# Kernel optimization log

Measured on AMD Instinct MI355X. Metric: run time of the kernel, lower is better.

## Reference

```python
import jax, jax.numpy as jnp
import numpy as np

NFFT = 512
SHIFT = 160
EPS = 1e-07
LOG10 = float(np.log(10.0))


def setup_inputs() -> dict:
    key = jax.random.key(0)
    x = jax.random.normal(key, (32, 1, 96512), dtype=jnp.float32)
    n = np.arange(NFFT)
    ang = 2.0 * np.pi * np.outer(n, n) / NFFT  # [k, n]
    W_real = np.cos(ang).astype(np.float32)
    W_imag = (-np.sin(ang)).astype(np.float32)
    return {"x": x, "W_real": jnp.asarray(W_real), "W_imag": jnp.asarray(W_imag)}


def reference(x, W_real, W_imag):
    # x: [B, C, T]; W_real/W_imag: [nfft, nfft] DFT basis (kernel k over taps n)
    B, C, T = x.shape
    n_frames = (T - NFFT) // SHIFT + 1
    # strided frame extraction == Conv1d(stride=SHIFT, kernel=NFFT) unfolding
    idx = jnp.arange(n_frames)[:, None] * SHIFT + jnp.arange(NFFT)[None, :]  # [F, N]
    frames = x[:, :, idx]  # [B, C, F, N]
    real = jnp.einsum('bcfn,kn->bckf', frames, W_real)  # [B, C, nfft, F]
    imag = jnp.einsum('bcfn,kn->bckf', frames, W_imag)
    # mode == 'log': log10 of magnitude spectrogram (with epsilon inside sqrt)
    fft = jnp.log(jnp.sqrt(real * real + imag * imag + EPS)) / LOG10
    fft = fft[:, :, : NFFT // 2, :]  # keep lower half of spectrum
    # normalize_feature: zero-mean, unit-std over frequency axis (biased std)
    mean = jnp.mean(fft, axis=2, keepdims=True)
    std = jnp.std(fft, axis=2, keepdims=True)
    return (fft - mean) / (std + EPS)
```

## Files before the change

kernel.cpp:

```cpp
#include <hip/hip_runtime.h>
#include <stdint.h>

#define TLEN    96512
#define NBATCH  32
#define KOUT    256
#define SHIFT   160
#define NFRAMES 601
#define FT      76
#define NTILES  8
#define NKS     16
#define EPSF    1e-7f

typedef _Float16 f16;
typedef _Float16 half8 __attribute__((ext_vector_type(8)));
typedef float f32x16 __attribute__((ext_vector_type(16)));

#define SPAN       ((FT - 1) * SHIFT + 256)
#define UNITS      (SPAN / 8)
#define PLANE_B    24576
#define LDS_RED    104768
#define LDS_STAT   (LDS_RED + 6144)
#define LDS_TOTAL  (LDS_STAT + 768)

__global__ __launch_bounds__(256) void split_w_kernel(
    const float* __restrict__ Wr, const float* __restrict__ Wi,
    f16* __restrict__ wsW)
{
    int id   = blockIdx.x * 256 + threadIdx.x;
    int lane = id & 63;
    int hl   = (id >> 6) & 1;
    int ri   = (id >> 7) & 1;
    int ks   = (id >> 8) & 15;
    int J    = (id >> 12) & 3;
    int par  = (id >> 14) & 1;
    int l31  = lane & 31, lhi = lane >> 5;
    int k = 2 * (J * 32 + l31) + par;
    int n = ks * 16 + lhi * 8;
    const float* src = (ri ? Wi : Wr) + k * 512 + n;
    f16 v[8];
    #pragma unroll
    for (int j = 0; j < 8; ++j) {
        float xv = src[j];
        f16 h = (f16)xv;
        v[j] = hl ? (f16)(xv - (float)h) : h;
    }
    int c = ((par * 4 + J) * 16 + ks) * 4 + ri * 2 + hl;
    *(half8*)(wsW + (size_t)c * 512 + (l31 * 2 + lhi) * 8) = *(half8*)v;
}

__device__ __forceinline__ void load_a(half8 (&a)[2][2],
    const f16* __restrict__ wsW, int par, int J, int laneoff, int ks)
{
    #pragma unroll
    for (int ri = 0; ri < 2; ++ri)
      #pragma unroll
      for (int hl = 0; hl < 2; ++hl) {
          int c = ((par * 4 + J) * 16 + ks) * 4 + ri * 2 + hl;
          a[ri][hl] = *(const half8*)(wsW + (size_t)c * 512 + laneoff);
      }
}

__device__ __forceinline__ void load_b(half8 (&bb)[3][2],
    const char* smem, int par, int l31, int lhi, int ks)
{
    #pragma unroll
    for (int nf = 0; nf < 3; ++nf)
      #pragma unroll
      for (int hl = 0; hl < 2; ++hl) {
          int u  = (nf * 32 + l31) * 20 + ks * 2 + lhi;
          int up = u ^ ((u >> 3) & 7);
          bb[nf][hl] = *(const half8*)(smem + (par * 2 + hl) * PLANE_B + up * 16);
      }
}

__device__ __forceinline__ void do_mfma(f32x16 (&acc)[3][2],
    const half8 (&a)[2][2], const half8 (&bb)[3][2])
{
    #pragma unroll
    for (int nf = 0; nf < 3; ++nf)
      #pragma unroll
      for (int ri = 0; ri < 2; ++ri) {
          acc[nf][ri] = __builtin_amdgcn_mfma_f32_32x32x16_f16(
              a[ri][0], bb[nf][0], acc[nf][ri], 0, 0, 0);
          acc[nf][ri] = __builtin_amdgcn_mfma_f32_32x32x16_f16(
              a[ri][0], bb[nf][1], acc[nf][ri], 0, 0, 0);
          acc[nf][ri] = __builtin_amdgcn_mfma_f32_32x32x16_f16(
              a[ri][1], bb[nf][0], acc[nf][ri], 0, 0, 0);
      }
}

__global__ __launch_bounds__(512, 2) void dft_mfma_kernel(
    const f16* __restrict__ wsW, const float* __restrict__ x,
    float* __restrict__ out)
{
    __shared__ uint4 smem4[LDS_TOTAL / 16];
    char* smem = (char*)smem4;

    const int tid  = threadIdx.x;
    const int lane = tid & 63;
    const int w    = tid >> 6;
    const int l31  = lane & 31;
    const int lhi  = lane >> 5;
    const int b    = blockIdx.y;
    const int f0   = blockIdx.x * FT;
    const int par  = w & 1;
    const int J    = w >> 1;
    const int laneoff = (l31 * 2 + lhi) * 8;

    half8 a0[2][2], a1[2][2], b0[3][2], b1[3][2];
    load_a(a0, wsW, par, J, laneoff, 0);

    {
        const float* __restrict__ xb = x + (size_t)b * TLEN;
        const int t0 = f0 * SHIFT;
        for (int u = tid; u < UNITS; u += 512) {
            int t = t0 + u * 8;
            float va[8], vb[8];
            if (t + 264 <= TLEN) {
                float4 p0 = *(const float4*)(xb + t);
                float4 p1 = *(const float4*)(xb + t + 4);
                float4 q0 = *(const float4*)(xb + t + 256);
                float4 q1 = *(const float4*)(xb + t + 260);
                va[0]=p0.x; va[1]=p0.y; va[2]=p0.z; va[3]=p0.w;
                va[4]=p1.x; va[5]=p1.y; va[6]=p1.z; va[7]=p1.w;
                vb[0]=q0.x; vb[1]=q0.y; vb[2]=q0.z; vb[3]=q0.w;
                vb[4]=q1.x; vb[5]=q1.y; vb[6]=q1.z; vb[7]=q1.w;
            } else {
                #pragma unroll
                for (int j = 0; j < 8; ++j) {
                    int ta = t + j, tb = t + 256 + j;
                    va[j] = (ta < TLEN) ? xb[ta] : 0.f;
                    vb[j] = (tb < TLEN) ? xb[tb] : 0.f;
                }
            }
            f16 eh[8], el[8], oh[8], ol[8];
            #pragma unroll
            for (int j = 0; j < 8; ++j) {
                float E = va[j] + vb[j], O = va[j] - vb[j];
                eh[j] = (f16)E; el[j] = (f16)(E - (float)eh[j]);
                oh[j] = (f16)O; ol[j] = (f16)(O - (float)oh[j]);
            }
            int up = u ^ ((u >> 3) & 7);
            *(half8*)(smem + 0 * PLANE_B + up * 16) = *(half8*)eh;
            *(half8*)(smem + 1 * PLANE_B + up * 16) = *(half8*)el;
            *(half8*)(smem + 2 * PLANE_B + up * 16) = *(half8*)oh;
            *(half8*)(smem + 3 * PLANE_B + up * 16) = *(half8*)ol;
        }
    }
    __syncthreads();

    f32x16 acc[3][2] = {};
    load_b(b0, smem, par, l31, lhi, 0);

    #pragma unroll
    for (int ks2 = 0; ks2 < NKS; ks2 += 2) {
        load_a(a1, wsW, par, J, laneoff, ks2 + 1);
        load_b(b1, smem, par, l31, lhi, ks2 + 1);
        do_mfma(acc, a0, b0);
        int k2 = (ks2 + 2 < NKS) ? ks2 + 2 : NKS - 1;
        load_a(a0, wsW, par, J, laneoff, k2);
        load_b(b0, smem, par, l31, lhi, k2);
        do_mfma(acc, a1, b1);
    }

    const float C = 0.15051499783199057f;
    float lg[3][16];
    float s1[3] = {0.f, 0.f, 0.f}, s2[3] = {0.f, 0.f, 0.f};
    #pragma unroll
    for (int nf = 0; nf < 3; ++nf)
      #pragma unroll
      for (int r = 0; r < 16; ++r) {
          float re = acc[nf][0][r], im = acc[nf][1][r];
          float lv = C * __log2f(re * re + im * im + EPSF);
          lg[nf][r] = lv;
          s1[nf] += lv;
          s2[nf] += lv * lv;
      }
    #pragma unroll
    for (int nf = 0; nf < 3; ++nf) {
        s1[nf] += __shfl_xor(s1[nf], 32);
        s2[nf] += __shfl_xor(s2[nf], 32);
    }
    float2* red = (float2*)(smem + LDS_RED);
    if (lane < 32) {
        #pragma unroll
        for (int nf = 0; nf < 3; ++nf)
            red[(w * 3 + nf) * 32 + l31] = make_float2(s1[nf], s2[nf]);
    }
    __syncthreads();
    float* stat = (float*)(smem + LDS_STAT);
    if (tid < 96) {
        float S1 = 0.f, S2 = 0.f;
        int nf = tid >> 5, c = tid & 31;
        #pragma unroll
        for (int ww = 0; ww < 8; ++ww) {
            float2 p = red[(ww * 3 + nf) * 32 + c];
            S1 += p.x; S2 += p.y;
        }
        float mean = S1 * (1.f / 256.f);
        float var  = fmaxf(S2 * (1.f / 256.f) - mean * mean, 0.f);
        stat[tid]      = mean;
        stat[96 + tid] = 1.f / (__builtin_sqrtf(var) + EPSF);
    }
    __syncthreads();

    #pragma unroll
    for (int nf = 0; nf < 3; ++nf) {
        int fl = nf * 32 + l31;
        int f  = f0 + fl;
        if (fl >= FT || f >= NFRAMES) continue;
        float mean = stat[fl], rstd = stat[96 + fl];
        #pragma unroll
        for (int r = 0; r < 16; ++r) {
            int k = 2 * (J * 32 + (r & 3) + 8 * (r >> 2) + 4 * lhi) + par;
            out[((size_t)b * KOUT + k) * NFRAMES + f] = (lg[nf][r] - mean) * rstd;
        }
    }
}

extern "C" void kernel_launch(void* const* d_in, const int* in_sizes, int n_in,
                              void* d_out, int out_size, void* d_ws, size_t ws_size,
                              hipStream_t stream) {
    const float* x  = (const float*)d_in[0];
    const float* Wr = (const float*)d_in[1];
    const float* Wi = (const float*)d_in[2];
    float* out = (float*)d_out;

    f16* wsW = (f16*)d_ws;

    split_w_kernel<<<128, 256, 0, stream>>>(Wr, Wi, wsW);

    dim3 grid(NTILES, NBATCH);
    dft_mfma_kernel<<<grid, 512, 0, stream>>>(wsW, x, out);
}
```

Baseline: 33.92 us.

## Shrink frame tile to 32 for more blocks and occupancy, simplify MFMA loop

The frame tile per block drops from 76 (three 32-wide N fragments, padded to 96) to 32, so the grid grows from 8x32 to 19x32 blocks. LDS per block shrinks and launch bounds rise to 4 blocks per CU. The aim is better CU coverage with less padding waste, plus higher occupancy to hide latency. The explicit double-buffered A/B prefetch is replaced by a simple unrolled loop with s_setprio around the MFMAs, and split_w is restructured so each thread writes both the high and low halves. In exchange, each block reloads the A (W) fragments for fewer frames, so W traffic grows and there is more overlapping x staging per frame.

```diff
diff --git a/kernel.cpp b/kernel.cpp
--- a/kernel.cpp
+++ b/kernel.cpp
@@ -6,8 +6,8 @@
 #define KOUT    256
 #define SHIFT   160
 #define NFRAMES 601
-#define FT      76
-#define NTILES  8
+#define FT      32
+#define NTILES  19
 #define NKS     16
 #define EPSF    1e-7f
 
@@ -17,79 +17,59 @@
 
 #define SPAN       ((FT - 1) * SHIFT + 256)
 #define UNITS      (SPAN / 8)
-#define PLANE_B    24576
-#define LDS_RED    104768
-#define LDS_STAT   (LDS_RED + 6144)
-#define LDS_TOTAL  (LDS_STAT + 768)
+#define PLANE_B    (UNITS * 16)
+#define LDS_RED    (4 * PLANE_B)
+#define LDS_STAT   (LDS_RED + 2048)
+#define LDS_TOTAL  (LDS_STAT + 256)
 
 __global__ __launch_bounds__(256) void split_w_kernel(
     const float* __restrict__ Wr, const float* __restrict__ Wi,
     f16* __restrict__ wsW)
 {
-    int id   = blockIdx.x * 256 + threadIdx.x;
-    int lane = id & 63;
-    int hl   = (id >> 6) & 1;
-    int ri   = (id >> 7) & 1;
-    int ks   = (id >> 8) & 15;
-    int J    = (id >> 12) & 3;
-    int par  = (id >> 14) & 1;
-    int l31  = lane & 31, lhi = lane >> 5;
-    int k = 2 * (J * 32 + l31) + par;
-    int n = ks * 16 + lhi * 8;
-    const float* src = (ri ? Wi : Wr) + k * 512 + n;
-    f16 v[8];
+    int id = blockIdx.x * 256 + threadIdx.x;
+    int n8 = id & 31;
+    int k  = (id >> 5) & 255;
+    int ri = (id >> 13) & 1;
+    const float* src = (ri ? Wi : Wr) + k * 512 + n8 * 8;
+    f16 h[8], l[8];
     #pragma unroll
     for (int j = 0; j < 8; ++j) {
-        float xv = src[j];
-        f16 h = (f16)xv;
-        v[j] = hl ? (f16)(xv - (float)h) : h;
-    }
-    int c = ((par * 4 + J) * 16 + ks) * 4 + ri * 2 + hl;
-    *(half8*)(wsW + (size_t)c * 512 + (l31 * 2 + lhi) * 8) = *(half8*)v;
+        float v = src[j];
+        h[j] = (f16)v;
+        l[j] = (f16)(v - (float)h[j]);
+    }
+    int par = k & 1, kk = k >> 1;
+    int l31 = kk & 31, J = kk >> 5;
+    int ks  = n8 >> 1, lhi = n8 & 1;
+    int c0  = ((par * 4 + J) * 16 + ks) * 4 + ri * 2;
+    size_t off = (size_t)(l31 * 2 + lhi) * 8;
+    *(half8*)(wsW + (size_t)(c0 + 0) * 512 + off) = *(half8*)h;
+    *(half8*)(wsW + (size_t)(c0 + 1) * 512 + off) = *(half8*)l;
 }
 
 __device__ __forceinline__ void load_a(half8 (&a)[2][2],
-    const f16* __restrict__ wsW, int par, int J, int laneoff, int ks)
+    const f16* __restrict__ wsW, int cbase, int laneoff, int ks)
 {
     #pragma unroll
     for (int ri = 0; ri < 2; ++ri)
       #pragma unroll
       for (int hl = 0; hl < 2; ++hl) {
-          int c = ((par * 4 + J) * 16 + ks) * 4 + ri * 2 + hl;
+          int c = cbase + ks * 4 + ri * 2 + hl;
           a[ri][hl] = *(const half8*)(wsW + (size_t)c * 512 + laneoff);
       }
 }
 
-__device__ __forceinline__ void load_b(half8 (&bb)[3][2],
-    const char* smem, int par, int l31, int lhi, int ks)
-{
-    #pragma unroll
-    for (int nf = 0; nf < 3; ++nf)
-      #pragma unroll
-      for (int hl = 0; hl < 2; ++hl) {
-          int u  = (nf * 32 + l31) * 20 + ks * 2 + lhi;
-          int up = u ^ ((u >> 3) & 7);
-          bb[nf][hl] = *(const half8*)(smem + (par * 2 + hl) * PLANE_B + up * 16);
-      }
-}
-
-__device__ __forceinline__ void do_mfma(f32x16 (&acc)[3][2],
-    const half8 (&a)[2][2], const half8 (&bb)[3][2])
-{
-    #pragma unroll
-    for (int nf = 0; nf < 3; ++nf)
-      #pragma unroll
-      for (int ri = 0; ri < 2; ++ri) {
-          acc[nf][ri] = __builtin_amdgcn_mfma_f32_32x32x16_f16(
-              a[ri][0], bb[nf][0], acc[nf][ri], 0, 0, 0);
-          acc[nf][ri] = __builtin_amdgcn_mfma_f32_32x32x16_f16(
-              a[ri][0], bb[nf][1], acc[nf][ri], 0, 0, 0);
-          acc[nf][ri] = __builtin_amdgcn_mfma_f32_32x32x16_f16(
-              a[ri][1], bb[nf][0], acc[nf][ri], 0, 0, 0);
-      }
-}
-
-__global__ __launch_bounds__(512, 2) void dft_mfma_kernel(
+__device__ __forceinline__ void load_b(half8 (&bb)[2],
+    const char* smem, int par, int ubase, int ks)
+{
+    int u  = ubase + ks * 2;
+    int up = u ^ ((u >> 3) & 3);
+    #pragma unroll
+    for (int hl = 0; hl < 2; ++hl)
+        bb[hl] = *(const half8*)(smem + (par * 2 + hl) * PLANE_B + up * 16);
+}
+
+__global__ __launch_bounds__(512, 4) void dft_mfma_kernel(
     const f16* __restrict__ wsW, const float* __restrict__ x,
     float* __restrict__ out)
 {
@@ -105,10 +85,9 @@
     const int f0   = blockIdx.x * FT;
     const int par  = w & 1;
     const int J    = w >> 1;
+    const int cbase   = (par * 4 + J) * 64;
     const int laneoff = (l31 * 2 + lhi) * 8;
-
-    half8 a0[2][2], a1[2][2], b0[3][2], b1[3][2];
-    load_a(a0, wsW, par, J, laneoff, 0);
+    const int ubase   = l31 * 20 + lhi;
 
     {
         const float* __restrict__ xb = x + (size_t)b * TLEN;
@@ -140,7 +119,7 @@
                 eh[j] = (f16)E; el[j] = (f16)(E - (float)eh[j]);
                 oh[j] = (f16)O; ol[j] = (f16)(O - (float)oh[j]);
             }
-            int up = u ^ ((u >> 3) & 7);
+            int up = u ^ ((u >> 3) & 3);
             *(half8*)(smem + 0 * PLANE_B + up * 16) = *(half8*)eh;
             *(half8*)(smem + 1 * PLANE_B + up * 16) = *(half8*)el;
             *(half8*)(smem + 2 * PLANE_B + up * 16) = *(half8*)oh;
@@ -149,71 +128,67 @@
     }
     __syncthreads();
 
-    f32x16 acc[3][2] = {};
-    load_b(b0, smem, par, l31, lhi, 0);
-
-    #pragma unroll
-    for (int ks2 = 0; ks2 < NKS; ks2 += 2) {
-        load_a(a1, wsW, par, J, laneoff, ks2 + 1);
-        load_b(b1, smem, par, l31, lhi, ks2 + 1);
-        do_mfma(acc, a0, b0);
-        int k2 = (ks2 + 2 < NKS) ? ks2 + 2 : NKS - 1;
-        load_a(a0, wsW, par, J, laneoff, k2);
-        load_b(b0, smem, par, l31, lhi, k2);
-        do_mfma(acc, a1, b1);
+    f32x16 acc[2] = {};
+
+    #pragma unroll 4
+    for (int ks = 0; ks < NKS; ++ks) {
+        half8 a[2][2], bb[2];
+        load_a(a, wsW, cbase, laneoff, ks);
+        load_b(bb, smem, par, ubase, ks);
+
+        __builtin_amdgcn_s_setprio(1);
+        #pragma unroll
+        for (int ri = 0; ri < 2; ++ri) {
+            acc[ri] = __builtin_amdgcn_mfma_f32_32x32x16_f16(
+                a[ri][0], bb[0], acc[ri], 0, 0, 0);
+            acc[ri] = __builtin_amdgcn_mfma_f32_32x32x16_f16(
+                a[ri][0], bb[1], acc[ri], 0, 0, 0);
+            acc[ri] = __builtin_amdgcn_mfma_f32_32x32x16_f16(
+                a[ri][1], bb[0], acc[ri], 0, 0, 0);
+        }
+        __builtin_amdgcn_s_setprio(0);
     }
 
     const float C = 0.15051499783199057f;
-    float lg[3][16];
-    float s1[3] = {0.f, 0.f, 0.f}, s2[3] = {0.f, 0.f, 0.f};
-    #pragma unroll
-    for (int nf = 0; nf < 3; ++nf)
-      #pragma unroll
-      for (int r = 0; r < 16; ++r) {
-          float re = acc[nf][0][r], im = acc[nf][1][r];
-          float lv = C * __log2f(re * re + im * im + EPSF);
-          lg[nf][r] = lv;
-          s1[nf] += lv;
-          s2[nf] += lv * lv;
-      }
-    #pragma unroll
-    for (int nf = 0; nf < 3; ++nf) {
-        s1[nf] += __shfl_xor(s1[nf], 32);
-        s2[nf] += __shfl_xor(s2[nf], 32);
-    }
+    float lg[16];
+    float s1 = 0.f, s2 = 0.f;
+    #pragma unroll
+    for (int r = 0; r < 16; ++r) {
+        float re = acc[0][r], im = acc[1][r];
+        float lv = C * __log2f(re * re + im * im + EPSF);
+        lg[r] = lv;
+        s1 += lv;
+        s2 += lv * lv;
+    }
+    s1 += __shfl_xor(s1, 32);
+    s2 += __shfl_xor(s2, 32);
+
     float2* red = (float2*)(smem + LDS_RED);
-    if (lane < 32) {
-        #pragma unroll
-        for (int nf = 0; nf < 3; ++nf)
-            red[(w * 3 + nf) * 32 + l31] = make_float2(s1[nf], s2[nf]);
-    }
+    if (lane < 32)
+        red[w * 32 + l31] = make_float2(s1, s2);
     __syncthreads();
     float* stat = (float*)(smem + LDS_STAT);
-    if (tid < 96) {
+    if (tid < 32) {
         float S1 = 0.f, S2 = 0.f;
-        int nf = tid >> 5, c = tid & 31;
         #pragma unroll
         for (int ww = 0; ww < 8; ++ww) {
-            float2 p = red[(ww * 3 + nf) * 32 + c];
+            float2 p = red[ww * 32 + tid];
             S1 += p.x; S2 += p.y;
         }
         float mean = S1 * (1.f / 256.f);
         float var  = fmaxf(S2 * (1.f / 256.f) - mean * mean, 0.f);
         stat[tid]      = mean;
-        stat[96 + tid] = 1.f / (__builtin_sqrtf(var) + EPSF);
+        stat[32 + tid] = 1.f / (__builtin_sqrtf(var) + EPSF);
     }
     __syncthreads();
 
-    #pragma unroll
-    for (int nf = 0; nf < 3; ++nf) {
-        int fl = nf * 32 + l31;
-        int f  = f0 + fl;
-        if (fl >= FT || f >= NFRAMES) continue;
-        float mean = stat[fl], rstd = stat[96 + fl];
+    const int f = f0 + l31;
+    if (f < NFRAMES) {
+        float mean = stat[l31], rstd = stat[32 + l31];
         #pragma unroll
         for (int r = 0; r < 16; ++r) {
             int k = 2 * (J * 32 + (r & 3) + 8 * (r >> 2) + 4 * lhi) + par;
-            out[((size_t)b * KOUT + k) * NFRAMES + f] = (lg[nf][r] - mean) * rstd;
+            out[((size_t)b * KOUT + k) * NFRAMES + f] = (lg[r] - mean) * rstd;
         }
     }
 }
@@ -228,7 +203,7 @@
 
     f16* wsW = (f16*)d_ws;
 
-    split_w_kernel<<<128, 256, 0, stream>>>(Wr, Wi, wsW);
+    split_w_kernel<<<64, 256, 0, stream>>>(Wr, Wi, wsW);
 
     dim3 grid(NTILES, NBATCH);
     dft_mfma_kernel<<<grid, 512, 0, stream>>>(wsW, x, out);
```

Measured after the change: 35.86 us. +5.7%, slower.

## Stage output through LDS for coalesced stores, raise MFMA priority, merge W split

Applied to the files above, without the earlier changes.

The epilogue now writes normalized values into a per-wave LDS patch and then stores contiguous frame rows per frequency, instead of scattering strided single-float stores. The MFMA block is wrapped in s_setprio to favour matrix issue over other waves. The weight split kernel now computes high and low halves in one thread and writes both, which halves its grid and avoids reading W twice. The LDS patch reuses the staging region after the barriers, so correctness depends on the input planes no longer being needed at that point.

```diff
diff --git a/kernel.cpp b/kernel.cpp
--- a/kernel.cpp
+++ b/kernel.cpp
@@ -26,26 +26,25 @@
     const float* __restrict__ Wr, const float* __restrict__ Wi,
     f16* __restrict__ wsW)
 {
-    int id   = blockIdx.x * 256 + threadIdx.x;
-    int lane = id & 63;
-    int hl   = (id >> 6) & 1;
-    int ri   = (id >> 7) & 1;
-    int ks   = (id >> 8) & 15;
-    int J    = (id >> 12) & 3;
-    int par  = (id >> 14) & 1;
-    int l31  = lane & 31, lhi = lane >> 5;
-    int k = 2 * (J * 32 + l31) + par;
-    int n = ks * 16 + lhi * 8;
-    const float* src = (ri ? Wi : Wr) + k * 512 + n;
-    f16 v[8];
+    int id = blockIdx.x * 256 + threadIdx.x;
+    int n8 = id & 31;
+    int k  = (id >> 5) & 255;
+    int ri = (id >> 13) & 1;
+    const float* src = (ri ? Wi : Wr) + k * 512 + n8 * 8;
+    f16 h[8], l[8];
     #pragma unroll
     for (int j = 0; j < 8; ++j) {
-        float xv = src[j];
-        f16 h = (f16)xv;
-        v[j] = hl ? (f16)(xv - (float)h) : h;
-    }
-    int c = ((par * 4 + J) * 16 + ks) * 4 + ri * 2 + hl;
-    *(half8*)(wsW + (size_t)c * 512 + (l31 * 2 + lhi) * 8) = *(half8*)v;
+        float v = src[j];
+        h[j] = (f16)v;
+        l[j] = (f16)(v - (float)h[j]);
+    }
+    int par = k & 1, kk = k >> 1;
+    int l31 = kk & 31, J = kk >> 5;
+    int ks  = n8 >> 1, lhi = n8 & 1;
+    int c0  = ((par * 4 + J) * 16 + ks) * 4 + ri * 2;
+    size_t off = (size_t)(l31 * 2 + lhi) * 8;
+    *(half8*)(wsW + (size_t)(c0 + 0) * 512 + off) = *(half8*)h;
+    *(half8*)(wsW + (size_t)(c0 + 1) * 512 + off) = *(half8*)l;
 }
 
 __device__ __forceinline__ void load_a(half8 (&a)[2][2],
@@ -76,6 +75,7 @@
 __device__ __forceinline__ void do_mfma(f32x16 (&acc)[3][2],
     const half8 (&a)[2][2], const half8 (&bb)[3][2])
 {
+    __builtin_amdgcn_s_setprio(1);
     #pragma unroll
     for (int nf = 0; nf < 3; ++nf)
       #pragma unroll
@@ -87,6 +87,7 @@
           acc[nf][ri] = __builtin_amdgcn_mfma_f32_32x32x16_f16(
               a[ri][1], bb[nf][0], acc[nf][ri], 0, 0, 0);
       }
+    __builtin_amdgcn_s_setprio(0);
 }
 
 __global__ __launch_bounds__(512, 2) void dft_mfma_kernel(
@@ -204,16 +205,27 @@
     }
     __syncthreads();
 
+    float* patch = (float*)smem + w * (32 * 96);
     #pragma unroll
     for (int nf = 0; nf < 3; ++nf) {
         int fl = nf * 32 + l31;
-        int f  = f0 + fl;
-        if (fl >= FT || f >= NFRAMES) continue;
         float mean = stat[fl], rstd = stat[96 + fl];
         #pragma unroll
         for (int r = 0; r < 16; ++r) {
-            int k = 2 * (J * 32 + (r & 3) + 8 * (r >> 2) + 4 * lhi) + par;
-            out[((size_t)b * KOUT + k) * NFRAMES + f] = (lg[nf][r] - mean) * rstd;
+            int kloc = (r & 3) + 8 * (r >> 2) + 4 * lhi;
+            patch[kloc * 96 + fl] = (lg[nf][r] - mean) * rstd;
+        }
+    }
+    #pragma unroll 8
+    for (int kloc = 0; kloc < 32; ++kloc) {
+        int kg = 2 * (J * 32 + kloc) + par;
+        float* dst = out + ((size_t)b * KOUT + kg) * NFRAMES + f0;
+        float v0 = patch[kloc * 96 + lane];
+        if (f0 + lane < NFRAMES)
+            dst[lane] = v0;
+        if (lane < FT - 64 && f0 + 64 + lane < NFRAMES) {
+            float v1 = patch[kloc * 96 + 64 + lane];
+            dst[64 + lane] = v1;
         }
     }
 }
@@ -228,7 +240,7 @@
 
     f16* wsW = (f16*)d_ws;
 
-    split_w_kernel<<<128, 256, 0, stream>>>(Wr, Wi, wsW);
+    split_w_kernel<<<64, 256, 0, stream>>>(Wr, Wi, wsW);
 
     dim3 grid(NTILES, NBATCH);
     dft_mfma_kernel<<<grid, 512, 0, stream>>>(wsW, x, out);
```

New measurement: 35.52 us. +4.7%, slower.
